# Kernel tuning notes

Measured on AMD Instinct MI355X. Metric: run time of the kernel, lower is better.

## Reference

```python
import jax, jax.numpy as jnp
import numpy as np

B, S, D, H, KD, VD, HID, L, V, OUTN = 16, 512, 512, 8, 64, 64, 2048, 4, 32000, 128
EPS = 1e-5


def _layer_norm(x, g, b):
    m = jnp.mean(x, axis=-1, keepdims=True)
    v = jnp.mean(jnp.square(x - m), axis=-1, keepdims=True)
    return (x - m) * jax.lax.rsqrt(v + EPS) * g + b


def _pos_encoding(seq_len, d_model):
    pos = jnp.arange(seq_len, dtype=jnp.float32)[:, None]
    div = jnp.exp(jnp.arange(0, d_model, 2, dtype=jnp.float32) * (-np.log(10000.0) / d_model))
    pe = jnp.zeros((seq_len, d_model), dtype=jnp.float32)
    pe = pe.at[:, 0::2].set(jnp.sin(pos * div))
    pe = pe.at[:, 1::2].set(jnp.cos(pos * div))
    return pe


def setup_inputs() -> dict:
    key = jax.random.key(0)
    ks = jax.random.split(key, 32)
    s = 0.02
    n = jax.random.normal
    inp = {
        "enc_inputs": jax.random.randint(ks[0], (B, S), 0, V, dtype=jnp.int32),
        "emb": n(ks[1], (V, D), jnp.float32) * s,
        # stacked per-layer params, leading dim = L
        "Wq": n(ks[2], (L, D, H * KD), jnp.float32) * s,
        "bq": jnp.zeros((L, H * KD), jnp.float32),
        "Wk": n(ks[3], (L, D, H * KD), jnp.float32) * s,
        "bk": jnp.zeros((L, H * KD), jnp.float32),
        "Wv": n(ks[4], (L, D, H * VD), jnp.float32) * s,
        "bv": jnp.zeros((L, H * VD), jnp.float32),
        "Wo": n(ks[5], (L, H * VD, D), jnp.float32) * s,
        "bo": jnp.zeros((L, D), jnp.float32),
        "ln1_g": jnp.ones((L, D), jnp.float32),
        "ln1_b": jnp.zeros((L, D), jnp.float32),
        "W1": n(ks[6], (L, D, HID), jnp.float32) * s,   # conv1d k=1 == linear
        "b1": jnp.zeros((L, HID), jnp.float32),
        "W2": n(ks[7], (L, HID, D), jnp.float32) * s,
        "b2": jnp.zeros((L, D), jnp.float32),
        "ln2_g": jnp.ones((L, D), jnp.float32),
        "ln2_b": jnp.zeros((L, D), jnp.float32),
        # flatten head created inside torch forward: [S*D, 128]
        "Wf": n(ks[8], (S * D, OUTN), jnp.float32) * s,
        "bf": jnp.zeros((OUTN,), jnp.float32),
        "Wout": n(ks[9], (OUTN, 1), jnp.float32) * s,
        "bout": jnp.zeros((1,), jnp.float32),
    }
    return inp


def _encoder(enc_inputs, emb, Wq, bq, Wk, bk, Wv, bv, Wo, bo, ln1_g, ln1_b,
             W1, b1, W2, b2, ln2_g, ln2_b, Wf, bf, Wout, bout):
    x = emb[enc_inputs] + _pos_encoding(S, D)[None, :, :]          # [B,S,D]
    pad = (enc_inputs == 0)[:, None, None, :]                      # [B,1,1,S]
    scale = 1.0 / np.sqrt(D)                                       # note: sqrt(embed_dim), as in source
    for l in range(L):
        # multi-head attention
        q = (x @ Wq[l] + bq[l]).reshape(B, S, H, KD)
        k = (x @ Wk[l] + bk[l]).reshape(B, S, H, KD)
        v = (x @ Wv[l] + bv[l]).reshape(B, S, H, VD)
        scores = jnp.einsum('bqhd,bkhd->bhqk', q, k) * scale
        scores = jnp.where(pad, -1e9, scores)
        attn = jax.nn.softmax(scores, axis=-1)
        ctx = jnp.einsum('bhqk,bkhd->bqhd', attn, v).reshape(B, S, H * VD)
        x = _layer_norm(ctx @ Wo[l] + bo[l] + x, ln1_g[l], ln1_b[l])
        # position-wise FFN (conv1d kernel_size=1)
        h = jax.nn.relu(x @ W1[l] + b1[l])
        x = _layer_norm(h @ W2[l] + b2[l] + x, ln2_g[l], ln2_b[l])
    flat = x.reshape(B, S * D)
    features = flat @ Wf + bf                                      # [B,128]
    y_score = jax.nn.sigmoid(features @ Wout + bout)               # [B,1]
    y_pred = jnp.round(y_score)
    return y_score, y_pred, features


def reference(enc_inputs, emb, Wq, bq, Wk, bk, Wv, bv, Wo, bo, ln1_g, ln1_b,
              W1, b1, W2, b2, ln2_g, ln2_b, Wf, bf, Wout, bout):
    return _encoder(enc_inputs, emb, Wq, bq, Wk, bk, Wv, bv, Wo, bo, ln1_g, ln1_b,
                    W1, b1, W2, b2, ln2_g, ln2_b, Wf, bf, Wout, bout)
```

## Files before the change

### kernel.cpp

```cpp
#include <hip/hip_runtime.h>
#include <hip/hip_bf16.h>
#include <math.h>

typedef unsigned short ushort_t;
typedef __attribute__((ext_vector_type(8))) short bf16x8;
typedef __attribute__((ext_vector_type(4))) float f32x4;

#define SCALE_QK 0.04419417382415922f
#define PE_C 0.017988946039015986f

__device__ __forceinline__ void g2lds16(const void* g, void* l) {
    __builtin_amdgcn_global_load_lds(
        (const __attribute__((address_space(1))) unsigned int*)g,
        (__attribute__((address_space(3))) unsigned int*)l,
        16, 0, 0);
}
__device__ __forceinline__ ushort_t f2bs(float v) {
    __hip_bfloat16 h = __float2bfloat16(v);
    return *reinterpret_cast<ushort_t*>(&h);
}
__device__ __forceinline__ float bs2f(ushort_t v) {
    return __uint_as_float(((unsigned int)v) << 16);
}

template<int BM, int BN, bool RELU, bool VT, bool STATS>
__global__ __launch_bounds__(256) void gemm2(
    const ushort_t* __restrict__ A, const ushort_t* __restrict__ B,
    const float* __restrict__ bias, const ushort_t* __restrict__ resb,
    ushort_t* __restrict__ C, float2* __restrict__ part,
    ushort_t* __restrict__ vt, int K, int lda, int ldb, int ldc)
{
    constexpr int MI = BM / 32, NJ = BN / 32;
    __shared__ ushort_t As[BM * 64];
    __shared__ ushort_t Bs[BN * 64];

    const int t = threadIdx.x;
    const int lane = t & 63, w = t >> 6;
    const int l16 = lane & 15, quad = lane >> 4;
    const int r8 = lane >> 3;
    const int kg = ((lane & 7) ^ r8) << 3;
    const int wm = (w >> 1) * (BM / 2);
    const int wn = (w & 1) * (BN / 2);

    const int m0 = blockIdx.y * BM, n0 = blockIdx.x * BN;

    f32x4 acc[MI][NJ];
    #pragma unroll
    for (int i = 0; i < MI; i++)
        #pragma unroll
        for (int j = 0; j < NJ; j++)
            acc[i][j] = (f32x4){0.f, 0.f, 0.f, 0.f};

    for (int k0 = 0; k0 < K; k0 += 64) {
        #pragma unroll
        for (int ii = 0; ii < BM / 32; ii++) {
            int rbase = w * (BM / 4) + ii * 8;
            g2lds16(A + (size_t)(m0 + rbase + r8) * lda + k0 + kg, &As[rbase * 64]);
        }
        #pragma unroll
        for (int ii = 0; ii < BN / 32; ii++) {
            int rbase = w * (BN / 4) + ii * 8;
            g2lds16(B + (size_t)(n0 + rbase + r8) * ldb + k0 + kg, &Bs[rbase * 64]);
        }
        __syncthreads();

        #pragma unroll
        for (int tt = 0; tt < 2; tt++) {
            bf16x8 af[MI], bf[NJ];
            #pragma unroll
            for (int i = 0; i < MI; i++) {
                int row = wm + i * 16 + l16;
                af[i] = *(const bf16x8*)&As[row * 64 + ((((tt << 2) + quad) ^ (row & 7)) << 3)];
            }
            #pragma unroll
            for (int j = 0; j < NJ; j++) {
                int row = wn + j * 16 + l16;
                bf[j] = *(const bf16x8*)&Bs[row * 64 + ((((tt << 2) + quad) ^ (row & 7)) << 3)];
            }
            #pragma unroll
            for (int i = 0; i < MI; i++)
                #pragma unroll
                for (int j = 0; j < NJ; j++)
                    acc[i][j] = __builtin_amdgcn_mfma_f32_16x16x32_bf16(
                        af[i], bf[j], acc[i][j], 0, 0, 0);
        }
        __syncthreads();
    }

    if (VT && n0 >= 1024) {
        #pragma unroll
        for (int i = 0; i < MI; i++) {
            int mbase = m0 + wm + i * 16 + quad * 4;
            int b = mbase >> 9, s = mbase & 511;
            #pragma unroll
            for (int j = 0; j < NJ; j++) {
                int n = n0 + wn + j * 16 + l16;
                int hv = n - 1024;
                int h = hv >> 6, vd = hv & 63;
                float bv = bias[n];
                ushort4 pk;
                pk.x = f2bs(acc[i][j][0] + bv);
                pk.y = f2bs(acc[i][j][1] + bv);
                pk.z = f2bs(acc[i][j][2] + bv);
                pk.w = f2bs(acc[i][j][3] + bv);
                *(ushort4*)&vt[((size_t)((b << 3) + h)) * 32768 + (size_t)vd * 512 + s] = pk;
            }
        }
        return;
    }

    #pragma unroll
    for (int i = 0; i < MI; i++) {
        float rs[4] = {0.f, 0.f, 0.f, 0.f}, rq[4] = {0.f, 0.f, 0.f, 0.f};
        #pragma unroll
        for (int j = 0; j < NJ; j++) {
            int n = n0 + wn + j * 16 + l16;
            float bv = bias ? bias[n] : 0.f;
            #pragma unroll
            for (int r = 0; r < 4; r++) {
                int m = m0 + wm + i * 16 + quad * 4 + r;
                float v = acc[i][j][r] + bv;
                if (resb) v += bs2f(resb[(size_t)m * ldc + n]);
                if (RELU) v = fmaxf(v, 0.f);
                C[(size_t)m * ldc + n] = f2bs(v);
                if (STATS) { rs[r] += v; rq[r] += v * v; }
            }
        }
        if (STATS) {
            #pragma unroll
            for (int r = 0; r < 4; r++) {
                float s = rs[r], q = rq[r];
                #pragma unroll
                for (int off = 1; off < 16; off <<= 1) {
                    s += __shfl_xor(s, off);
                    q += __shfl_xor(q, off);
                }
                if (l16 == 0) {
                    int m = m0 + wm + i * 16 + quad * 4 + r;
                    part[(size_t)m * 16 + blockIdx.x * 2 + (w & 1)] = make_float2(s, q);
                }
            }
        }
    }
}

__global__ __launch_bounds__(256) void flash_attn(
    ushort_t* __restrict__ QKV, const ushort_t* __restrict__ Vt,
    const int* __restrict__ tok)
{
    __shared__ ushort_t Qs[128 * 64];
    __shared__ ushort_t Ks[128 * 64];
    __shared__ ushort_t Vts[64 * 128];
    __shared__ ushort_t Ps[128 * 128];

    const int bh = blockIdx.y;
    const int b = bh >> 3, h = bh & 7;
    const int q0 = blockIdx.x * 128;
    const int t = threadIdx.x;
    const int lane = t & 63, w = t >> 6;
    const int l16 = lane & 15, quad = lane >> 4;
    const int wm = w * 32;
    const size_t rowbase = (size_t)b * 512;

    {
        int r8 = lane >> 3;
        int kg = (lane & 7) ^ r8;
        #pragma unroll
        for (int ii = 0; ii < 4; ii++) {
            int rb = w * 32 + ii * 8;
            g2lds16(QKV + (rowbase + q0 + rb + r8) * 1536 + h * 64 + kg * 8,
                    &Qs[rb * 64]);
        }
    }

    f32x4 accO[2][4];
    #pragma unroll
    for (int i = 0; i < 2; i++)
        #pragma unroll
        for (int jv = 0; jv < 4; jv++)
            accO[i][jv] = (f32x4){0.f, 0.f, 0.f, 0.f};
    float lrow[2][4];
    #pragma unroll
    for (int i = 0; i < 2; i++)
        #pragma unroll
        for (int r = 0; r < 4; r++) lrow[i][r] = 0.f;

    for (int kc = 0; kc < 4; kc++) {
        __syncthreads();
        {
            int r8 = lane >> 3;
            int kg = (lane & 7) ^ r8;
            #pragma unroll
            for (int ii = 0; ii < 4; ii++) {
                int rb = w * 32 + ii * 8;
                g2lds16(QKV + (rowbase + kc * 128 + rb + r8) * 1536 + 512 + h * 64 + kg * 8,
                        &Ks[rb * 64]);
            }
        }
        {
            int v4 = lane >> 4;
            #pragma unroll
            for (int ii = 0; ii < 4; ii++) {
                int vb = w * 16 + ii * 4;
                int vd = vb + v4;
                int kg = (lane & 15) ^ (vd & 15);
                g2lds16(Vt + (size_t)bh * 32768 + (size_t)vd * 512 + kc * 128 + kg * 8,
                        &Vts[vb * 128]);
            }
        }
        float maskv[8];
        #pragma unroll
        for (int j = 0; j < 8; j++)
            maskv[j] = (tok[b * 512 + kc * 128 + j * 16 + l16] == 0) ? -1e9f : 0.f;

        __syncthreads();

        f32x4 sacc[2][8];
        #pragma unroll
        for (int i = 0; i < 2; i++)
            #pragma unroll
            for (int j = 0; j < 8; j++)
                sacc[i][j] = (f32x4){0.f, 0.f, 0.f, 0.f};
        #pragma unroll
        for (int tt = 0; tt < 2; tt++) {
            bf16x8 aq[2], bk8[8];
            #pragma unroll
            for (int i = 0; i < 2; i++) {
                int row = wm + i * 16 + l16;
                aq[i] = *(const bf16x8*)&Qs[row * 64 + (((tt << 2) + quad) ^ (row & 7)) * 8];
            }
            #pragma unroll
            for (int j = 0; j < 8; j++) {
                int row = j * 16 + l16;
                bk8[j] = *(const bf16x8*)&Ks[row * 64 + (((tt << 2) + quad) ^ (row & 7)) * 8];
            }
            #pragma unroll
            for (int i = 0; i < 2; i++)
                #pragma unroll
                for (int j = 0; j < 8; j++)
                    sacc[i][j] = __builtin_amdgcn_mfma_f32_16x16x32_bf16(
                        aq[i], bk8[j], sacc[i][j], 0, 0, 0);
        }

        #pragma unroll
        for (int i = 0; i < 2; i++)
            #pragma unroll
            for (int j = 0; j < 8; j++)
                #pragma unroll
                for (int r = 0; r < 4; r++) {
                    float p = __expf(fmaf(sacc[i][j][r], SCALE_QK, maskv[j]));
                    sacc[i][j][r] = p;
                    lrow[i][r] += p;
                }

        #pragma unroll
        for (int i = 0; i < 2; i++)
            #pragma unroll
            for (int j = 0; j < 8; j++) {
                int col = j * 16 + l16;
                int colc = col >> 3, csub = col & 7;
                #pragma unroll
                for (int r = 0; r < 4; r++) {
                    int row = wm + i * 16 + quad * 4 + r;
                    Ps[row * 128 + ((colc ^ (row & 15)) << 3) + csub] = f2bs(sacc[i][j][r]);
                }
            }

        #pragma unroll
        for (int tt = 0; tt < 4; tt++) {
            bf16x8 ap[2], bv8[4];
            #pragma unroll
            for (int i = 0; i < 2; i++) {
                int row = wm + i * 16 + l16;
                ap[i] = *(const bf16x8*)&Ps[row * 128 + ((((tt << 2) + quad)) ^ (row & 15)) * 8];
            }
            #pragma unroll
            for (int jv = 0; jv < 4; jv++) {
                int vd = jv * 16 + l16;
                bv8[jv] = *(const bf16x8*)&Vts[vd * 128 + (((tt << 2) + quad) ^ (vd & 15)) * 8];
            }
            #pragma unroll
            for (int i = 0; i < 2; i++)
                #pragma unroll
                for (int jv = 0; jv < 4; jv++)
                    accO[i][jv] = __builtin_amdgcn_mfma_f32_16x16x32_bf16(
                        ap[i], bv8[jv], accO[i][jv], 0, 0, 0);
        }
    }

    #pragma unroll
    for (int i = 0; i < 2; i++)
        #pragma unroll
        for (int r = 0; r < 4; r++) {
            float s = lrow[i][r];
            #pragma unroll
            for (int off = 1; off < 16; off <<= 1)
                s += __shfl_xor(s, off);
            float inv = 1.f / s;
            int row = q0 + wm + i * 16 + quad * 4 + r;
            #pragma unroll
            for (int jv = 0; jv < 4; jv++) {
                int vd = jv * 16 + l16;
                QKV[(rowbase + row) * 1536 + h * 64 + vd] = f2bs(accO[i][jv][r] * inv);
            }
        }
}

__global__ __launch_bounds__(256) void transpose_cvt(
    const float* __restrict__ in, __hip_bfloat16* __restrict__ out,
    int R, int Cc, long long inz, long long outz)
{
    in  += blockIdx.z * inz;
    out += blockIdx.z * outz;
    __shared__ float tile[32][33];
    int c0 = blockIdx.x * 32, r0 = blockIdx.y * 32;
    int tx = threadIdx.x & 31, ty = threadIdx.x >> 5;
    #pragma unroll
    for (int i = 0; i < 4; i++)
        tile[ty + i * 8][tx] = in[(size_t)(r0 + ty + i * 8) * Cc + c0 + tx];
    __syncthreads();
    #pragma unroll
    for (int i = 0; i < 4; i++)
        out[(size_t)(c0 + ty + i * 8) * R + r0 + tx] =
            __float2bfloat16(tile[tx][ty + i * 8]);
}

__global__ __launch_bounds__(256) void concat_bias(const float* __restrict__ bq,
                                                   const float* __restrict__ bk,
                                                   const float* __restrict__ bv,
                                                   float* __restrict__ bqkv) {
    int idx = blockIdx.x * 256 + threadIdx.x;
    if (idx >= 4 * 1536) return;
    int l = idx / 1536, n = idx - l * 1536;
    float v = (n < 512) ? bq[l * 512 + n]
            : (n < 1024) ? bk[l * 512 + n - 512]
                         : bv[l * 512 + n - 1024];
    bqkv[idx] = v;
}

__global__ __launch_bounds__(256) void embed_pe_b(const int* __restrict__ tok,
                                                  const float* __restrict__ emb,
                                                  __hip_bfloat16* __restrict__ xb) {
    int idx = blockIdx.x * 256 + threadIdx.x;
    int d  = idx & 511;
    int bs = idx >> 9;
    int s  = bs & 511;
    int t  = tok[bs];
    float freq  = expf(-(float)(d & ~1) * PE_C);
    float angle = (float)s * freq;
    float pe    = (d & 1) ? cosf(angle) : sinf(angle);
    xb[idx] = __float2bfloat16(emb[(size_t)t * 512 + d] + pe);
}

__global__ __launch_bounds__(256) void ln_stats(const ushort_t* __restrict__ Cpre,
                                                const float2* __restrict__ part,
                                                const float* __restrict__ g,
                                                const float* __restrict__ b,
                                                ushort_t* __restrict__ Xb) {
    long long row = blockIdx.x;
    int t = threadIdx.x;
    float s = 0.f, q = 0.f;
    if (t < 16) {
        float2 p = part[row * 16 + t];
        s = p.x; q = p.y;
    }
    #pragma unroll
    for (int off = 1; off < 16; off <<= 1) {
        s += __shfl_xor(s, off);
        q += __shfl_xor(q, off);
    }
    __shared__ float mv[2];
    if (t == 0) {
        float mean = s * (1.f / 512.f);
        float var = q * (1.f / 512.f) - mean * mean;
        mv[0] = mean;
        mv[1] = rsqrtf(var + 1e-5f);
    }
    __syncthreads();
    float mean = mv[0], r = mv[1];
    int c = t * 2;
    ushort2 u = *(const ushort2*)&Cpre[row * 512 + c];
    ushort2 o;
    o.x = f2bs((bs2f(u.x) - mean) * r * g[c]     + b[c]);
    o.y = f2bs((bs2f(u.y) - mean) * r * g[c + 1] + b[c + 1]);
    *(ushort2*)&Xb[row * 512 + c] = o;
}

__global__ __launch_bounds__(256) void feat_partial(const ushort_t* __restrict__ Xb,
                                                    const float* __restrict__ Wf,
                                                    float* __restrict__ FbP) {
    int slice = blockIdx.x;
    int k0 = slice * 512;
    __shared__ float Xs[16][512];
    int t = threadIdx.x;
    for (int i = t; i < 2048; i += 256) {
        int b = i >> 7, c4 = (i & 127) * 4;
        ushort4 u = *(const ushort4*)&Xb[(size_t)b * 262144 + k0 + c4];
        Xs[b][c4 + 0] = bs2f(u.x);
        Xs[b][c4 + 1] = bs2f(u.y);
        Xs[b][c4 + 2] = bs2f(u.z);
        Xs[b][c4 + 3] = bs2f(u.w);
    }
    __syncthreads();
    int n4 = (t & 31) * 4;
    int kh = t >> 5;
    float4 acc[16];
    #pragma unroll
    for (int b = 0; b < 16; b++) acc[b] = (float4){0.f, 0.f, 0.f, 0.f};
    for (int kk4 = 0; kk4 < 16; kk4++) {
        int kb = kh * 64 + kk4 * 4;
        float4 w0 = *(const float4*)&Wf[(size_t)(k0 + kb + 0) * 128 + n4];
        float4 w1 = *(const float4*)&Wf[(size_t)(k0 + kb + 1) * 128 + n4];
        float4 w2 = *(const float4*)&Wf[(size_t)(k0 + kb + 2) * 128 + n4];
        float4 w3 = *(const float4*)&Wf[(size_t)(k0 + kb + 3) * 128 + n4];
        #pragma unroll
        for (int b = 0; b < 16; b++) {
            float4 xq = *(const float4*)&Xs[b][kb];
            acc[b].x += xq.x * w0.x + xq.y * w1.x + xq.z * w2.x + xq.w * w3.x;
            acc[b].y += xq.x * w0.y + xq.y * w1.y + xq.z * w2.y + xq.w * w3.y;
            acc[b].z += xq.x * w0.z + xq.y * w1.z + xq.z * w2.z + xq.w * w3.z;
            acc[b].w += xq.x * w0.w + xq.y * w1.w + xq.z * w2.w + xq.w * w3.w;
        }
    }
    float* dst = FbP + ((size_t)slice * 8 + kh) * 2048;
    #pragma unroll
    for (int b = 0; b < 16; b++)
        *(float4*)&dst[b * 128 + n4] = acc[b];
}

__global__ __launch_bounds__(256) void feat_reduce(const float* __restrict__ FbP,
                                                   float* __restrict__ Fb) {
    int idx = blockIdx.x * 256 + threadIdx.x;
    int j0 = blockIdx.y * 128;
    float s = 0.f;
    for (int j = 0; j < 128; j++) s += FbP[(size_t)(j0 + j) * 2048 + idx];
    atomicAdd(&Fb[idx], s);
}

__global__ __launch_bounds__(256) void head_kernel(const float* __restrict__ feat,
                                                   const float* __restrict__ bfv,
                                                   const float* __restrict__ Wo2,
                                                   const float* __restrict__ bo2,
                                                   float* __restrict__ out) {
    __shared__ float f[2048];
    int t = threadIdx.x;
    for (int i = t; i < 2048; i += 256) {
        float v = feat[i] + bfv[i & 127];
        f[i] = v;
        out[32 + i] = v;
    }
    __syncthreads();
    if (t < 16) {
        float zv = bo2[0];
        for (int n = 0; n < 128; n++) zv = fmaf(f[t * 128 + n], Wo2[n], zv);
        float ys = 1.f / (1.f + expf(-zv));
        out[t] = ys;
        out[16 + t] = rintf(ys);
    }
}

extern "C" void kernel_launch(void* const* d_in, const int* in_sizes, int n_in,
                              void* d_out, int out_size, void* d_ws, size_t ws_size,
                              hipStream_t stream) {
    const int*   enc  = (const int*)  d_in[0];
    const float* emb  = (const float*)d_in[1];
    const float* Wq   = (const float*)d_in[2];
    const float* bq   = (const float*)d_in[3];
    const float* Wk   = (const float*)d_in[4];
    const float* bk   = (const float*)d_in[5];
    const float* Wv   = (const float*)d_in[6];
    const float* bv   = (const float*)d_in[7];
    const float* Wo   = (const float*)d_in[8];
    const float* bo   = (const float*)d_in[9];
    const float* g1   = (const float*)d_in[10];
    const float* be1  = (const float*)d_in[11];
    const float* W1   = (const float*)d_in[12];
    const float* b1f  = (const float*)d_in[13];
    const float* W2   = (const float*)d_in[14];
    const float* b2f  = (const float*)d_in[15];
    const float* g2   = (const float*)d_in[16];
    const float* be2  = (const float*)d_in[17];
    const float* Wf   = (const float*)d_in[18];
    const float* bf   = (const float*)d_in[19];
    const float* Wout = (const float*)d_in[20];
    const float* bout = (const float*)d_in[21];
    float* out = (float*)d_out;

    char* ws = (char*)d_ws;
    ushort_t* Cpre = (ushort_t*) (ws + 0);
    ushort_t* Xb   = (ushort_t*) (ws + 16777216);
    ushort_t* QKV  = (ushort_t*) (ws + 25165824);
    ushort_t* Vt   = (ushort_t*) (ws + 50331648);
    ushort_t* S    = (ushort_t*) (ws + 58720256);
    ushort_t* WqkvT= (ushort_t*) (ws + 92274688);
    ushort_t* WoT  = (ushort_t*) (ws + 98566144);
    ushort_t* W1T  = (ushort_t*) (ws + 100663296);
    ushort_t* W2T  = (ushort_t*) (ws + 109051904);
    float*    bqkv = (float*)    (ws + 117440512);
    float*    Fb   = (float*)    (ws + 117465088);
    float2*   part = (float2*)   (ws + 117473280);
    float*    FbP  = (float*)    (ws + 25165824);

    typedef __hip_bfloat16 bf16;

    transpose_cvt<<<dim3(16, 16, 4), 256, 0, stream>>>(Wq, (bf16*)WqkvT,            512, 512,  262144, 786432);
    transpose_cvt<<<dim3(16, 16, 4), 256, 0, stream>>>(Wk, (bf16*)(WqkvT + 262144), 512, 512,  262144, 786432);
    transpose_cvt<<<dim3(16, 16, 4), 256, 0, stream>>>(Wv, (bf16*)(WqkvT + 524288), 512, 512,  262144, 786432);
    transpose_cvt<<<dim3(16, 16, 4), 256, 0, stream>>>(Wo, (bf16*)WoT,              512, 512,  262144, 262144);
    transpose_cvt<<<dim3(64, 16, 4), 256, 0, stream>>>(W1, (bf16*)W1T,              512, 2048, 1048576, 1048576);
    transpose_cvt<<<dim3(16, 64, 4), 256, 0, stream>>>(W2, (bf16*)W2T,              2048, 512, 1048576, 1048576);
    concat_bias<<<24, 256, 0, stream>>>(bq, bk, bv, bqkv);

    embed_pe_b<<<16384, 256, 0, stream>>>(enc, emb, (bf16*)Xb);

    for (int l = 0; l < 4; l++) {
        gemm2<128, 128, false, true, false><<<dim3(12, 64), 256, 0, stream>>>(
            Xb, WqkvT + (size_t)l * 786432, bqkv + l * 1536, nullptr,
            QKV, nullptr, Vt, 512, 512, 512, 1536);

        flash_attn<<<dim3(4, 128), 256, 0, stream>>>(QKV, Vt, enc);

        gemm2<128, 64, false, false, true><<<dim3(8, 64), 256, 0, stream>>>(
            QKV, WoT + (size_t)l * 262144, bo + l * 512, Xb,
            Cpre, part, nullptr, 512, 1536, 512, 512);
        ln_stats<<<8192, 256, 0, stream>>>(Cpre, part, g1 + l * 512, be1 + l * 512, Xb);

        gemm2<128, 128, true, false, false><<<dim3(16, 64), 256, 0, stream>>>(
            Xb, W1T + (size_t)l * 1048576, b1f + l * 2048, nullptr,
            S, nullptr, nullptr, 512, 512, 512, 2048);
        gemm2<128, 64, false, false, true><<<dim3(8, 64), 256, 0, stream>>>(
            S, W2T + (size_t)l * 1048576, b2f + l * 512, Xb,
            Cpre, part, nullptr, 2048, 2048, 2048, 512);
        ln_stats<<<8192, 256, 0, stream>>>(Cpre, part, g2 + l * 512, be2 + l * 512, Xb);
    }

    hipMemsetAsync(Fb, 0, 2048 * sizeof(float), stream);
    feat_partial<<<512, 256, 0, stream>>>(Xb, Wf, FbP);
    feat_reduce<<<dim3(8, 32), 256, 0, stream>>>(FbP, Fb);
    head_kernel<<<1, 256, 0, stream>>>(Fb, bf, Wout, bout, out);
}
```

Measured before the change: 1.093 ms.

## Add 256x256-tile 8-wave GEMM kernel for QKV and FFN1 projections

```diff
diff --git a/kernel.cpp b/kernel.cpp
--- a/kernel.cpp
+++ b/kernel.cpp
@@ -142,6 +142,122 @@
             }
         }
     }
+}
+
+template<bool RELU, bool VT>
+__global__ __launch_bounds__(512, 2) void gemm8(
+    const ushort_t* __restrict__ A, const ushort_t* __restrict__ B,
+    const float* __restrict__ bias, ushort_t* __restrict__ C,
+    ushort_t* __restrict__ vt, int K, int lda, int ldb, int ldc)
+{
+    __shared__ ushort_t As[2][256 * 64];
+    __shared__ ushort_t Bs[2][256 * 64];
+
+    const int t = threadIdx.x;
+    const int lane = t & 63, w = t >> 6;
+    const int l16 = lane & 15, quad = lane >> 4;
+    const int r8 = lane >> 3;
+    const int kg = ((lane & 7) ^ r8) << 3;
+    const int wm = (w >> 2) * 128;
+    const int wn = (w & 3) * 64;
+    const int m0 = blockIdx.y * 256, n0 = blockIdx.x * 256;
+    const int NT = K >> 6;
+
+    f32x4 acc[8][4];
+    #pragma unroll
+    for (int i = 0; i < 8; i++)
+        #pragma unroll
+        for (int j = 0; j < 4; j++)
+            acc[i][j] = (f32x4){0.f, 0.f, 0.f, 0.f};
+
+    auto STAGE8 = [&](int kt, int bb) {
+        int k0 = kt << 6;
+        #pragma unroll
+        for (int ii = 0; ii < 4; ii++) {
+            int rbase = w * 32 + ii * 8;
+            g2lds16(A + (size_t)(m0 + rbase + r8) * lda + k0 + kg,
+                    &As[bb][rbase * 64]);
+            g2lds16(B + (size_t)(n0 + rbase + r8) * ldb + k0 + kg,
+                    &Bs[bb][rbase * 64]);
+        }
+    };
+
+    STAGE8(0, 0);
+    STAGE8(1, 1);
+
+    for (int kt = 0; kt < NT; kt++) {
+        const int bb = kt & 1;
+        if (kt < NT - 1)
+            asm volatile("s_waitcnt vmcnt(8)" ::: "memory");
+        else
+            asm volatile("s_waitcnt vmcnt(0)" ::: "memory");
+        __builtin_amdgcn_s_barrier();
+        asm volatile("" ::: "memory");
+
+        #pragma unroll
+        for (int tt = 0; tt < 2; tt++) {
+            bf16x8 af[8], bf[4];
+            #pragma unroll
+            for (int i = 0; i < 8; i++) {
+                int row = wm + i * 16 + l16;
+                af[i] = *(const bf16x8*)&As[bb][row * 64 + ((((tt << 2) + quad) ^ (row & 7)) << 3)];
+            }
+            #pragma unroll
+            for (int j = 0; j < 4; j++) {
+                int row = wn + j * 16 + l16;
+                bf[j] = *(const bf16x8*)&Bs[bb][row * 64 + ((((tt << 2) + quad) ^ (row & 7)) << 3)];
+            }
+            #pragma unroll
+            for (int i = 0; i < 8; i++)
+                #pragma unroll
+                for (int j = 0; j < 4; j++)
+                    acc[i][j] = __builtin_amdgcn_mfma_f32_16x16x32_bf16(
+                        af[i], bf[j], acc[i][j], 0, 0, 0);
+        }
+
+        asm volatile("" ::: "memory");
+        __builtin_amdgcn_s_barrier();
+        asm volatile("" ::: "memory");
+        if (kt + 2 < NT)
+            STAGE8(kt + 2, bb);
+    }
+
+    if (VT && n0 >= 1024) {
+        #pragma unroll
+        for (int i = 0; i < 8; i++) {
+            int mbase = m0 + wm + i * 16 + quad * 4;
+            int b = mbase >> 9, s = mbase & 511;
+            #pragma unroll
+            for (int j = 0; j < 4; j++) {
+                int n = n0 + wn + j * 16 + l16;
+                int hv = n - 1024;
+                int h = hv >> 6, vd = hv & 63;
+                float bv = bias[n];
+                ushort4 pk;
+                pk.x = f2bs(acc[i][j][0] + bv);
+                pk.y = f2bs(acc[i][j][1] + bv);
+                pk.z = f2bs(acc[i][j][2] + bv);
+                pk.w = f2bs(acc[i][j][3] + bv);
+                *(ushort4*)&vt[((size_t)((b << 3) + h)) * 32768 + (size_t)vd * 512 + s] = pk;
+            }
+        }
+        return;
+    }
+
+    #pragma unroll
+    for (int i = 0; i < 8; i++)
+        #pragma unroll
+        for (int j = 0; j < 4; j++) {
+            int n = n0 + wn + j * 16 + l16;
+            float bv = bias[n];
+            #pragma unroll
+            for (int r = 0; r < 4; r++) {
+                int m = m0 + wm + i * 16 + quad * 4 + r;
+                float v = acc[i][j][r] + bv;
+                if (RELU) v = fmaxf(v, 0.f);
+                C[(size_t)m * ldc + n] = f2bs(v);
+            }
+        }
 }
 
 __global__ __launch_bounds__(256) void flash_attn(
@@ -514,9 +630,9 @@
     embed_pe_b<<<16384, 256, 0, stream>>>(enc, emb, (bf16*)Xb);
 
     for (int l = 0; l < 4; l++) {
-        gemm2<128, 128, false, true, false><<<dim3(12, 64), 256, 0, stream>>>(
-            Xb, WqkvT + (size_t)l * 786432, bqkv + l * 1536, nullptr,
-            QKV, nullptr, Vt, 512, 512, 512, 1536);
+        gemm8<false, true><<<dim3(6, 32), 512, 0, stream>>>(
+            Xb, WqkvT + (size_t)l * 786432, bqkv + l * 1536,
+            QKV, Vt, 512, 512, 512, 1536);
 
         flash_attn<<<dim3(4, 128), 256, 0, stream>>>(QKV, Vt, enc);
 
@@ -525,9 +641,9 @@
             Cpre, part, nullptr, 512, 1536, 512, 512);
         ln_stats<<<8192, 256, 0, stream>>>(Cpre, part, g1 + l * 512, be1 + l * 512, Xb);
 
-        gemm2<128, 128, true, false, false><<<dim3(16, 64), 256, 0, stream>>>(
-            Xb, W1T + (size_t)l * 1048576, b1f + l * 2048, nullptr,
-            S, nullptr, nullptr, 512, 512, 512, 2048);
+        gemm8<true, false><<<dim3(8, 32), 512, 0, stream>>>(
+            Xb, W1T + (size_t)l * 1048576, b1f + l * 2048,
+            S, nullptr, 512, 512, 512, 2048);
         gemm2<128, 64, false, false, true><<<dim3(8, 64), 256, 0, stream>>>(
             S, W2T + (size_t)l * 1048576, b2f + l * 512, Xb,
             Cpre, part, nullptr, 2048, 2048, 2048, 512);
```

Measured after the change: 1.057 ms. -3.4%, faster.
